# Optimization experiments

Measured on AMD Instinct MI355X. Metric: run time of the kernel, lower is better.

Reference implementation:

```python
import jax, jax.numpy as jnp
import numpy as np

N = 384          # item_num (text regions)
TD = 768         # text hidden (bert-base)
VD = 768         # vision hidden (vit-base)
CD = TD + VD     # commu_dim = 1536
FF = 2048        # TransformerEncoderLayer default dim_feedforward
H = 4            # nhead
L = 2            # num_layers per encoder
EPS = 1e-5


def _enc_params(key, d, scale=0.02):
    ks = jax.random.split(key, 6)
    return dict(
        qkv_w=jax.random.normal(ks[0], (L, 3 * d, d), jnp.float32) * scale,
        qkv_b=jnp.zeros((L, 3 * d), jnp.float32),
        out_w=jax.random.normal(ks[1], (L, d, d), jnp.float32) * scale,
        out_b=jnp.zeros((L, d), jnp.float32),
        ln1_s=jnp.ones((L, d), jnp.float32),
        ln1_b=jnp.zeros((L, d), jnp.float32),
        ff1_w=jax.random.normal(ks[2], (L, FF, d), jnp.float32) * scale,
        ff1_b=jnp.zeros((L, FF), jnp.float32),
        ff2_w=jax.random.normal(ks[3], (L, d, FF), jnp.float32) * scale,
        ff2_b=jnp.zeros((L, d), jnp.float32),
        ln2_s=jnp.ones((L, d), jnp.float32),
        ln2_b=jnp.zeros((L, d), jnp.float32),
    )


def setup_inputs() -> dict:
    key = jax.random.key(0)
    k = jax.random.split(key, 6)
    inp = {
        'text_emb': jax.random.normal(k[0], (N, TD), jnp.float32),
        'vision_emb': jax.random.normal(k[1], (N, VD), jnp.float32),
        'gt_matrix': jax.random.randint(k[2], (N, N), 0, 2, jnp.int32),
    }
    for pref, kk, d in (('t_', k[3], TD), ('c_', k[4], CD)):
        for name, v in _enc_params(kk, d).items():
            inp[pref + name] = v
    inp['lin_w'] = jax.random.normal(k[5], (2, 2 * CD), jnp.float32) * 0.02
    inp['lin_b'] = jnp.zeros((2,), jnp.float32)
    return inp


def _ln(x, s, b):
    m = jnp.mean(x, -1, keepdims=True)
    v = jnp.mean((x - m) ** 2, -1, keepdims=True)
    return (x - m) * jax.lax.rsqrt(v + EPS) * s + b


def _encoder(x, qkv_w, qkv_b, out_w, out_b, ln1_s, ln1_b,
             ff1_w, ff1_b, ff2_w, ff2_b, ln2_s, ln2_b):
    # PyTorch post-norm TransformerEncoder, relu activation, eval mode (no dropout)
    d = x.shape[-1]
    hd = d // H
    for l in range(qkv_w.shape[0]):
        qkv = x @ qkv_w[l].T + qkv_b[l]
        q, kk, v = jnp.split(qkv, 3, axis=-1)
        q = q.reshape(-1, H, hd)
        kk = kk.reshape(-1, H, hd)
        v = v.reshape(-1, H, hd)
        scores = jnp.einsum('qhd,khd->hqk', q, kk) / jnp.sqrt(jnp.float32(hd))
        attn = jax.nn.softmax(scores, -1)
        o = jnp.einsum('hqk,khd->qhd', attn, v).reshape(-1, d)
        x = _ln(x + o @ out_w[l].T + out_b[l], ln1_s[l], ln1_b[l])
        h = jax.nn.relu(x @ ff1_w[l].T + ff1_b[l]) @ ff2_w[l].T + ff2_b[l]
        x = _ln(x + h, ln2_s[l], ln2_b[l])
    return x


def reference(text_emb, vision_emb, gt_matrix,
              t_qkv_w, t_qkv_b, t_out_w, t_out_b, t_ln1_s, t_ln1_b,
              t_ff1_w, t_ff1_b, t_ff2_w, t_ff2_b, t_ln2_s, t_ln2_b,
              c_qkv_w, c_qkv_b, c_out_w, c_out_b, c_ln1_s, c_ln1_b,
              c_ff1_w, c_ff1_b, c_ff2_w, c_ff2_b, c_ln2_s, c_ln2_b,
              lin_w, lin_b):
    te = _encoder(text_emb, t_qkv_w, t_qkv_b, t_out_w, t_out_b, t_ln1_s, t_ln1_b,
                  t_ff1_w, t_ff1_b, t_ff2_w, t_ff2_b, t_ln2_s, t_ln2_b)
    all_emb = jnp.concatenate([te, vision_emb], axis=1)  # [N, CD]
    all_emb = _encoder(all_emb, c_qkv_w, c_qkv_b, c_out_w, c_out_b, c_ln1_s, c_ln1_b,
                       c_ff1_w, c_ff1_b, c_ff2_w, c_ff2_b, c_ln2_s, c_ln2_b)
    # organize(): linear(cat(e_i, e_j)) decomposes exactly as e_i@Wa^T + e_j@Wb^T + b,
    # avoiding the O(N^2 * 2*CD) pair tensor while computing identical math.
    a = all_emb @ lin_w[:, :CD].T + lin_b      # [N, 2]
    c = all_emb @ lin_w[:, CD:].T              # [N, 2]
    logits = a[:, None, :] + c[None, :, :]     # [N, N, 2]
    probs = jax.nn.softmax(logits, -1)         # self.activate(self.linear(...))
    # classificaiton_loss: sum_i CrossEntropyLoss(probs[i], gt[i])  (CE takes probs as logits)
    ls = jax.nn.log_softmax(probs, -1)
    cell = -jnp.take_along_axis(ls, gt_matrix[..., None].astype(jnp.int32), axis=-1)[..., 0]
    cls_loss = jnp.sum(jnp.mean(cell, axis=1))
    # enter_exit_loss over first N-1 items
    link = probs[:, :, 1]
    ee_loss = jnp.sum(jnp.abs(link.sum(1)[:-1] + link.sum(0)[:-1] - 1.0))
    return probs, cls_loss, ee_loss
```

## Files before the change

### kernel.cpp

```cpp
#include <hip/hip_runtime.h>
#include <hip/hip_bf16.h>
#include <math.h>

#define NTOK 384
#define HEADS 4

typedef __attribute__((ext_vector_type(8))) short bf16x8;
typedef __attribute__((ext_vector_type(4))) float f32x4;

__device__ __forceinline__ unsigned short f2b(float f) {
    union { float f; unsigned int u; } v; v.f = f;
    unsigned int r = (v.u + 0x7fff + ((v.u >> 16) & 1)) >> 16;
    return (unsigned short)r;
}

__device__ __forceinline__ void g2l16(const void* g, void* l) {
    __builtin_amdgcn_global_load_lds(
        (const __attribute__((address_space(1))) unsigned int*)g,
        (__attribute__((address_space(3))) unsigned int*)l, 16, 0, 0);
}

__device__ __forceinline__ void stage64(
    const unsigned short* __restrict__ g, int row0, int k0, int ld,
    char* region, int wid, int lane)
{
    int c = wid * 64 + lane;
    int row = c >> 2, p = c & 3;
    int kc = (p - (row >> 1)) & 3;
    g2l16(g + (long)(row0 + row) * ld + k0 + kc * 8,
          region + (wid * 64) * 16);
}

__global__ __launch_bounds__(256, 4) void gemm64(
    const unsigned short* __restrict__ A, const unsigned short* __restrict__ B,
    const float* __restrict__ bias, void* __restrict__ Cv,
    int K, int lda, int ldb, int ldc,
    long sA, long sB, long sC, int relu, int out_bf16,
    unsigned short* __restrict__ vt, int dv2)
{
    __shared__ char smem[2][16384];
    A += (long)blockIdx.z * sA;
    B += (long)blockIdx.z * sB;
    const int t = threadIdx.x, lane = t & 63, wid = t >> 6;
    const int wm = wid >> 1, wn = wid & 1;
    const int r16 = lane & 15, quad = lane >> 4;
    const int row0 = blockIdx.y * 64, col0 = blockIdx.x * 64;

    f32x4 acc[2][2] = {};

    stage64(A, row0,  0, lda, smem[0],         wid, lane);
    stage64(A, row0, 32, lda, smem[0] +  4096, wid, lane);
    stage64(B, col0,  0, ldb, smem[0] +  8192, wid, lane);
    stage64(B, col0, 32, ldb, smem[0] + 12288, wid, lane);
    int buf = 0;

    for (int k0 = 0; k0 < K; k0 += 64) {
        __syncthreads();
        if (k0 + 64 < K) {
            stage64(A, row0, k0 + 64, lda, smem[buf ^ 1],         wid, lane);
            stage64(A, row0, k0 + 96, lda, smem[buf ^ 1] +  4096, wid, lane);
            stage64(B, col0, k0 + 64, ldb, smem[buf ^ 1] +  8192, wid, lane);
            stage64(B, col0, k0 + 96, ldb, smem[buf ^ 1] + 12288, wid, lane);
        }
        const char* cb = smem[buf];
        #pragma unroll
        for (int h = 0; h < 2; ++h) {
            bf16x8 af[2], bfv[2];
            #pragma unroll
            for (int rt = 0; rt < 2; ++rt) {
                int row = wm * 32 + rt * 16 + r16;
                int p = (quad + (row >> 1)) & 3;
                af[rt] = *reinterpret_cast<const bf16x8*>(
                    cb + h * 4096 + row * 64 + p * 16);
            }
            #pragma unroll
            for (int ct = 0; ct < 2; ++ct) {
                int col = wn * 32 + ct * 16 + r16;
                int p = (quad + (col >> 1)) & 3;
                bfv[ct] = *reinterpret_cast<const bf16x8*>(
                    cb + 8192 + h * 4096 + col * 64 + p * 16);
            }
            #pragma unroll
            for (int rt = 0; rt < 2; ++rt)
                #pragma unroll
                for (int ct = 0; ct < 2; ++ct)
                    acc[rt][ct] = __builtin_amdgcn_mfma_f32_16x16x32_bf16(
                        af[rt], bfv[ct], acc[rt][ct], 0, 0, 0);
        }
        buf ^= 1;
    }

    float* Cf = (float*)Cv;
    unsigned short* Cb = (unsigned short*)Cv;
    const long zoff = (long)blockIdx.z * sC;
    const int vwrite = (vt != nullptr) && (col0 >= dv2);
    #pragma unroll
    for (int rt = 0; rt < 2; ++rt) {
        #pragma unroll
        for (int ct = 0; ct < 2; ++ct) {
            f32x4 v = acc[rt][ct];
            int col = col0 + wn * 32 + ct * 16 + r16;
            float bi = bias ? bias[col] : 0.f;
            #pragma unroll
            for (int i = 0; i < 4; ++i) {
                v[i] += bi;
                if (relu) v[i] = fmaxf(v[i], 0.f);
            }
            int rbase = row0 + wm * 32 + rt * 16 + quad * 4;
            if (vwrite) {
                ushort4 p;
                p.x = f2b(v[0]); p.y = f2b(v[1]); p.z = f2b(v[2]); p.w = f2b(v[3]);
                *reinterpret_cast<ushort4*>(vt + (long)(col - dv2) * NTOK + rbase) = p;
            } else if (out_bf16) {
                #pragma unroll
                for (int i = 0; i < 4; ++i)
                    Cb[zoff + (long)(rbase + i) * ldc + col] = f2b(v[i]);
            } else {
                #pragma unroll
                for (int i = 0; i < 4; ++i)
                    Cf[zoff + (long)(rbase + i) * ldc + col] = v[i];
            }
        }
    }
}

#define WO0 0u
#define WO1 3538944u
#define WO2 4718592u
#define WO3 7864320u
#define WO4 11010048u
#define WO5 25165824u
#define WO6 29884416u
#define WO7 36175872u
#define WTOT 42467328u

__global__ __launch_bounds__(256) void convert_weights(
    const float* __restrict__ s0, const float* __restrict__ s1,
    const float* __restrict__ s2, const float* __restrict__ s3,
    const float* __restrict__ s4, const float* __restrict__ s5,
    const float* __restrict__ s6, const float* __restrict__ s7,
    unsigned short* __restrict__ dst)
{
    unsigned int e = (blockIdx.x * 256u + threadIdx.x) * 8u;
    if (e >= WTOT) return;
    const float* src; unsigned int local;
    if      (e < WO1) { src = s0; local = e - WO0; }
    else if (e < WO2) { src = s1; local = e - WO1; }
    else if (e < WO3) { src = s2; local = e - WO2; }
    else if (e < WO4) { src = s3; local = e - WO3; }
    else if (e < WO5) { src = s4; local = e - WO4; }
    else if (e < WO6) { src = s5; local = e - WO5; }
    else if (e < WO7) { src = s6; local = e - WO6; }
    else              { src = s7; local = e - WO7; }
    float4 v0 = *reinterpret_cast<const float4*>(src + local);
    float4 v1 = *reinterpret_cast<const float4*>(src + local + 4);
    uint4 o;
    o.x = (unsigned)f2b(v0.x) | ((unsigned)f2b(v0.y) << 16);
    o.y = (unsigned)f2b(v0.z) | ((unsigned)f2b(v0.w) << 16);
    o.z = (unsigned)f2b(v1.x) | ((unsigned)f2b(v1.y) << 16);
    o.w = (unsigned)f2b(v1.z) | ((unsigned)f2b(v1.w) << 16);
    *reinterpret_cast<uint4*>(dst + e) = o;
}

__global__ __launch_bounds__(64) void softmax_rows(
    const float* __restrict__ S, unsigned short* __restrict__ P, float scale)
{
    const float* p = S + (long)blockIdx.x * NTOK;
    unsigned short* q = P + (long)blockIdx.x * NTOK;
    const int t = threadIdx.x;
    float vals[6];
    float vmax = -1e30f;
    #pragma unroll
    for (int i = 0; i < 6; ++i) {
        vals[i] = p[t + i * 64] * scale;
        vmax = fmaxf(vmax, vals[i]);
    }
    for (int off = 32; off; off >>= 1) vmax = fmaxf(vmax, __shfl_down(vmax, off));
    vmax = __shfl(vmax, 0);
    float sum = 0.f;
    #pragma unroll
    for (int i = 0; i < 6; ++i) { vals[i] = __expf(vals[i] - vmax); sum += vals[i]; }
    for (int off = 32; off; off >>= 1) sum += __shfl_down(sum, off);
    sum = __shfl(sum, 0);
    float inv = 1.f / sum;
    #pragma unroll
    for (int i = 0; i < 6; ++i) q[t + i * 64] = f2b(vals[i] * inv);
}

__global__ __launch_bounds__(256) void add_ln(
    float* __restrict__ x, unsigned short* __restrict__ xb,
    const float* __restrict__ y,
    const float* __restrict__ s, const float* __restrict__ b, int d)
{
    float* xr = x + (long)blockIdx.x * d;
    unsigned short* xbr = xb + (long)blockIdx.x * d;
    const float* yr = y + (long)blockIdx.x * d;
    const int t = threadIdx.x;
    float s1 = 0.f, s2 = 0.f;
    for (int i = t; i < d; i += 256) {
        float v = xr[i] + yr[i];
        s1 += v; s2 += v * v;
    }
    for (int off = 32; off; off >>= 1) { s1 += __shfl_down(s1, off); s2 += __shfl_down(s2, off); }
    __shared__ float r1[4], r2[4];
    int w = t >> 6;
    if ((t & 63) == 0) { r1[w] = s1; r2[w] = s2; }
    __syncthreads();
    if (t == 0) {
        float a = 0.f, c = 0.f;
        for (int i = 0; i < 4; ++i) { a += r1[i]; c += r2[i]; }
        r1[0] = a; r2[0] = c;
    }
    __syncthreads();
    float mean = r1[0] / d;
    float var = r2[0] / d - mean * mean;
    float rstd = rsqrtf(var + 1e-5f);
    for (int i = t; i < d; i += 256) {
        float v = (xr[i] + yr[i] - mean) * rstd * s[i] + b[i];
        xr[i] = v;
        xbr[i] = f2b(v);
    }
}

__global__ void initx_k(const float* __restrict__ src, float* __restrict__ dst,
                        unsigned short* __restrict__ dstb, int n)
{
    int i = blockIdx.x * blockDim.x + threadIdx.x;
    if (i < n) { float v = src[i]; dst[i] = v; dstb[i] = f2b(v); }
}

__global__ void concat_k(const float* __restrict__ te, const float* __restrict__ ve,
                         float* __restrict__ all, unsigned short* __restrict__ allb)
{
    int i = blockIdx.x * blockDim.x + threadIdx.x;
    if (i >= NTOK * 1536) return;
    int r = i / 1536, c = i % 1536;
    float v = (c < 768) ? te[r * 768 + c] : ve[r * 768 + (c - 768)];
    all[i] = v;
    allb[i] = f2b(v);
}

__global__ __launch_bounds__(256) void head_ac(
    const float* __restrict__ all, const float* __restrict__ lin_w,
    const float* __restrict__ lin_b, float* __restrict__ a, float* __restrict__ c)
{
    const int i = blockIdx.x, t = threadIdx.x;
    const float* xr = all + (long)i * 1536;
    float s0 = 0.f, s1 = 0.f, s2 = 0.f, s3 = 0.f;
    for (int e = t; e < 1536; e += 256) {
        float v = xr[e];
        s0 += v * lin_w[e];
        s1 += v * lin_w[3072 + e];
        s2 += v * lin_w[1536 + e];
        s3 += v * lin_w[4608 + e];
    }
    for (int off = 32; off; off >>= 1) {
        s0 += __shfl_down(s0, off); s1 += __shfl_down(s1, off);
        s2 += __shfl_down(s2, off); s3 += __shfl_down(s3, off);
    }
    __shared__ float r[4][4];
    int w = t >> 6;
    if ((t & 63) == 0) { r[0][w] = s0; r[1][w] = s1; r[2][w] = s2; r[3][w] = s3; }
    __syncthreads();
    if (t == 0) {
        float t0 = 0.f, t1 = 0.f, t2 = 0.f, t3 = 0.f;
        for (int k = 0; k < 4; ++k) { t0 += r[0][k]; t1 += r[1][k]; t2 += r[2][k]; t3 += r[3][k]; }
        a[i * 2 + 0] = t0 + lin_b[0];
        a[i * 2 + 1] = t1 + lin_b[1];
        c[i * 2 + 0] = t2;
        c[i * 2 + 1] = t3;
    }
}

__global__ __launch_bounds__(384) void head_probs(
    const float* __restrict__ a, const float* __restrict__ c,
    const int* __restrict__ gt, float* __restrict__ probs,
    float* __restrict__ rowsum, float* __restrict__ rowcell)
{
    const int i = blockIdx.x, j = threadIdx.x;
    float l0 = a[i * 2 + 0] + c[j * 2 + 0];
    float l1 = a[i * 2 + 1] + c[j * 2 + 1];
    float m = fmaxf(l0, l1);
    float e0 = __expf(l0 - m), e1 = __expf(l1 - m);
    float inv = 1.f / (e0 + e1);
    float p0 = e0 * inv, p1 = e1 * inv;
    long base = ((long)i * NTOK + j) * 2;
    probs[base] = p0;
    probs[base + 1] = p1;
    float m2 = fmaxf(p0, p1);
    float z = m2 + __logf(__expf(p0 - m2) + __expf(p1 - m2));
    int g = gt[i * NTOK + j];
    float cell = z - (g ? p1 : p0);
    float cs = cell, ps = p1;
    for (int off = 32; off; off >>= 1) { cs += __shfl_down(cs, off); ps += __shfl_down(ps, off); }
    __shared__ float rc[6], rs[6];
    int w = j >> 6;
    if ((j & 63) == 0) { rc[w] = cs; rs[w] = ps; }
    __syncthreads();
    if (j == 0) {
        float csum = 0.f, psum = 0.f;
        for (int k = 0; k < 6; ++k) { csum += rc[k]; psum += rs[k]; }
        rowcell[i] = csum * (1.f / NTOK);
        rowsum[i] = psum;
    }
}

__global__ __launch_bounds__(64) void colsum_k(const float* __restrict__ probs,
                                               float* __restrict__ colsum)
{
    const int j = blockIdx.x, t = threadIdx.x;
    float s = 0.f;
    for (int i = t; i < NTOK; i += 64)
        s += probs[((long)i * NTOK + j) * 2 + 1];
    for (int off = 32; off; off >>= 1) s += __shfl_down(s, off);
    if (t == 0) colsum[j] = s;
}

__global__ __launch_bounds__(384) void finalize_k(
    const float* __restrict__ rowcell, const float* __restrict__ rowsum,
    const float* __restrict__ colsum, float* __restrict__ out)
{
    const int t = threadIdx.x;
    float cls = rowcell[t];
    float ee = (t < NTOK - 1) ? fabsf(rowsum[t] + colsum[t] - 1.f) : 0.f;
    for (int off = 32; off; off >>= 1) { cls += __shfl_down(cls, off); ee += __shfl_down(ee, off); }
    __shared__ float rc[6], re[6];
    int w = t >> 6;
    if ((t & 63) == 0) { rc[w] = cls; re[w] = ee; }
    __syncthreads();
    if (t == 0) {
        float a = 0.f, b = 0.f;
        for (int k = 0; k < 6; ++k) { a += rc[k]; b += re[k]; }
        out[NTOK * NTOK * 2 + 0] = a;
        out[NTOK * NTOK * 2 + 1] = b;
    }
}

static void run_encoder(float* x, unsigned short* xb, int d,
                        const unsigned short* wq, const unsigned short* wo,
                        const unsigned short* w1, const unsigned short* w2,
                        const float* qkv_b, const float* out_b,
                        const float* ln1_s, const float* ln1_b,
                        const float* ff1_b, const float* ff2_b,
                        const float* ln2_s, const float* ln2_b,
                        unsigned short* qkvb, float* sc, unsigned short* attnb,
                        unsigned short* vtb, unsigned short* ob,
                        unsigned short* t1b, float* t2,
                        hipStream_t stream)
{
    const int dq = 3 * d;
    const int hd = d / HEADS;
    const float scale = 1.0f / sqrtf((float)hd);
    for (int l = 0; l < 2; ++l) {
        gemm64<<<dim3(dq / 64, 6), 256, 0, stream>>>(
            xb, wq + (long)l * dq * d, qkv_b + l * dq, qkvb,
            d, d, d, dq, 0, 0, 0, 0, 1, vtb, 2 * d);
        gemm64<<<dim3(6, 6, HEADS), 256, 0, stream>>>(
            qkvb, qkvb + d, nullptr, sc,
            hd, dq, dq, NTOK, (long)hd, (long)hd, (long)NTOK * NTOK,
            0, 0, nullptr, 0);
        softmax_rows<<<HEADS * NTOK, 64, 0, stream>>>(sc, attnb, scale);
        gemm64<<<dim3(hd / 64, 6, HEADS), 256, 0, stream>>>(
            attnb, vtb, nullptr, ob,
            NTOK, NTOK, NTOK, d, (long)NTOK * NTOK, (long)hd * NTOK, (long)hd,
            0, 1, nullptr, 0);
        gemm64<<<dim3(d / 64, 6), 256, 0, stream>>>(
            ob, wo + (long)l * d * d, out_b + l * d, t2,
            d, d, d, d, 0, 0, 0, 0, 0, nullptr, 0);
        add_ln<<<NTOK, 256, 0, stream>>>(x, xb, t2, ln1_s + l * d, ln1_b + l * d, d);
        gemm64<<<dim3(2048 / 64, 6), 256, 0, stream>>>(
            xb, w1 + (long)l * 2048 * d, ff1_b + l * 2048, t1b,
            d, d, d, 2048, 0, 0, 0, 1, 1, nullptr, 0);
        gemm64<<<dim3(d / 64, 6), 256, 0, stream>>>(
            t1b, w2 + (long)l * d * 2048, ff2_b + l * d, t2,
            2048, 2048, 2048, d, 0, 0, 0, 0, 0, nullptr, 0);
        add_ln<<<NTOK, 256, 0, stream>>>(x, xb, t2, ln2_s + l * d, ln2_b + l * d, d);
    }
}

extern "C" void kernel_launch(void* const* d_in, const int* in_sizes, int n_in,
                              void* d_out, int out_size, void* d_ws, size_t ws_size,
                              hipStream_t stream)
{
    const float* text_emb   = (const float*)d_in[0];
    const float* vision_emb = (const float*)d_in[1];
    const int*   gt         = (const int*)  d_in[2];
    const float* t_qkv_w = (const float*)d_in[3];
    const float* t_qkv_b = (const float*)d_in[4];
    const float* t_out_w = (const float*)d_in[5];
    const float* t_out_b = (const float*)d_in[6];
    const float* t_ln1_s = (const float*)d_in[7];
    const float* t_ln1_b = (const float*)d_in[8];
    const float* t_ff1_w = (const float*)d_in[9];
    const float* t_ff1_b = (const float*)d_in[10];
    const float* t_ff2_w = (const float*)d_in[11];
    const float* t_ff2_b = (const float*)d_in[12];
    const float* t_ln2_s = (const float*)d_in[13];
    const float* t_ln2_b = (const float*)d_in[14];
    const float* c_qkv_w = (const float*)d_in[15];
    const float* c_qkv_b = (const float*)d_in[16];
    const float* c_out_w = (const float*)d_in[17];
    const float* c_out_b = (const float*)d_in[18];
    const float* c_ln1_s = (const float*)d_in[19];
    const float* c_ln1_b = (const float*)d_in[20];
    const float* c_ff1_w = (const float*)d_in[21];
    const float* c_ff1_b = (const float*)d_in[22];
    const float* c_ff2_w = (const float*)d_in[23];
    const float* c_ff2_b = (const float*)d_in[24];
    const float* c_ln2_s = (const float*)d_in[25];
    const float* c_ln2_b = (const float*)d_in[26];
    const float* lin_w   = (const float*)d_in[27];
    const float* lin_b   = (const float*)d_in[28];
    float* out = (float*)d_out;

    float* ws = (float*)d_ws;
    float* xt      = ws;
    float* all     = xt + 294912;
    float* t2      = all + 589824;
    float* sc      = t2 + 589824;
    float* abuf    = sc + 589824;
    float* cbuf    = abuf + 768;
    float* rowsum  = cbuf + 768;
    float* rowcell = rowsum + 384;
    float* colsum  = rowcell + 384;
    unsigned short* ub = (unsigned short*)(ws + 2067072);
    unsigned short* xtb   = ub;
    unsigned short* allb  = xtb + 294912;
    unsigned short* qkvb  = allb + 589824;
    unsigned short* attnb = qkvb + 1769472;
    unsigned short* vtb   = attnb + 589824;
    unsigned short* ob    = vtb + 589824;
    unsigned short* t1b   = ob + 589824;
    unsigned short* wb    = t1b + 786432;

    convert_weights<<<(WTOT / 8 + 255) / 256, 256, 0, stream>>>(
        t_qkv_w, t_out_w, t_ff1_w, t_ff2_w,
        c_qkv_w, c_out_w, c_ff1_w, c_ff2_w, wb);

    initx_k<<<(294912 + 255) / 256, 256, 0, stream>>>(text_emb, xt, xtb, 294912);
    run_encoder(xt, xtb, 768,
                wb + WO0, wb + WO1, wb + WO2, wb + WO3,
                t_qkv_b, t_out_b, t_ln1_s, t_ln1_b,
                t_ff1_b, t_ff2_b, t_ln2_s, t_ln2_b,
                qkvb, sc, attnb, vtb, ob, t1b, t2, stream);

    concat_k<<<(589824 + 255) / 256, 256, 0, stream>>>(xt, vision_emb, all, allb);
    run_encoder(all, allb, 1536,
                wb + WO4, wb + WO5, wb + WO6, wb + WO7,
                c_qkv_b, c_out_b, c_ln1_s, c_ln1_b,
                c_ff1_b, c_ff2_b, c_ln2_s, c_ln2_b,
                qkvb, sc, attnb, vtb, ob, t1b, t2, stream);

    head_ac<<<NTOK, 256, 0, stream>>>(all, lin_w, lin_b, abuf, cbuf);
    head_probs<<<NTOK, 384, 0, stream>>>(abuf, cbuf, gt, out, rowsum, rowcell);
    colsum_k<<<NTOK, 64, 0, stream>>>(out, colsum);
    finalize_k<<<1, 384, 0, stream>>>(rowcell, rowsum, colsum, out);
}
```

Measured before the change: 563.9 us.

## Triple-buffer GEMM LDS staging with explicit vmcnt waits

Changes the 64x64 bf16 GEMM from a double-buffered to a triple-buffered LDS pipeline, prefetching two k-tiles ahead. It replaces __syncthreads with targeted s_waitcnt vmcnt counts plus s_barrier, so the in-flight global-to-LDS loads for the next tile are not drained each iteration. LDS per block grows to 48KB and launch bounds drop from 4 to 3 blocks per CU, which may reduce occupancy.

```diff
diff --git a/kernel.cpp b/kernel.cpp
--- a/kernel.cpp
+++ b/kernel.cpp
@@ -31,14 +31,26 @@
           region + (wid * 64) * 16);
 }
 
-__global__ __launch_bounds__(256, 4) void gemm64(
+__device__ __forceinline__ void stage_tile(
+    const unsigned short* __restrict__ A, const unsigned short* __restrict__ B,
+    int row0, int col0, int k0, int lda, int ldb,
+    char* buf, int wid, int lane)
+{
+    stage64(A, row0, k0,      lda, buf,         wid, lane);
+    stage64(A, row0, k0 + 32, lda, buf +  4096, wid, lane);
+    stage64(B, col0, k0,      ldb, buf +  8192, wid, lane);
+    stage64(B, col0, k0 + 32, ldb, buf + 12288, wid, lane);
+    __builtin_amdgcn_sched_barrier(0);
+}
+
+__global__ __launch_bounds__(256, 3) void gemm64(
     const unsigned short* __restrict__ A, const unsigned short* __restrict__ B,
     const float* __restrict__ bias, void* __restrict__ Cv,
     int K, int lda, int ldb, int ldc,
     long sA, long sB, long sC, int relu, int out_bf16,
     unsigned short* __restrict__ vt, int dv2)
 {
-    __shared__ char smem[2][16384];
+    __shared__ char smem[3][16384];
     A += (long)blockIdx.z * sA;
     B += (long)blockIdx.z * sB;
     const int t = threadIdx.x, lane = t & 63, wid = t >> 6;
@@ -47,22 +59,24 @@
     const int row0 = blockIdx.y * 64, col0 = blockIdx.x * 64;
 
     f32x4 acc[2][2] = {};
-
-    stage64(A, row0,  0, lda, smem[0],         wid, lane);
-    stage64(A, row0, 32, lda, smem[0] +  4096, wid, lane);
-    stage64(B, col0,  0, ldb, smem[0] +  8192, wid, lane);
-    stage64(B, col0, 32, ldb, smem[0] + 12288, wid, lane);
-    int buf = 0;
-
-    for (int k0 = 0; k0 < K; k0 += 64) {
-        __syncthreads();
-        if (k0 + 64 < K) {
-            stage64(A, row0, k0 + 64, lda, smem[buf ^ 1],         wid, lane);
-            stage64(A, row0, k0 + 96, lda, smem[buf ^ 1] +  4096, wid, lane);
-            stage64(B, col0, k0 + 64, ldb, smem[buf ^ 1] +  8192, wid, lane);
-            stage64(B, col0, k0 + 96, ldb, smem[buf ^ 1] + 12288, wid, lane);
+    const int NT = K >> 6;
+
+    stage_tile(A, B, row0, col0, 0, lda, ldb, smem[0], wid, lane);
+    if (NT > 1)
+        stage_tile(A, B, row0, col0, 64, lda, ldb, smem[1], wid, lane);
+
+    int cur = 0, sb = 2;
+    for (int kt = 0; kt < NT; ++kt) {
+        if (kt + 1 < NT) asm volatile("s_waitcnt vmcnt(4)" ::: "memory");
+        else             asm volatile("s_waitcnt vmcnt(0) lgkmcnt(0)" ::: "memory");
+        __builtin_amdgcn_s_barrier();
+        if (kt + 2 < NT) {
+            stage_tile(A, B, row0, col0, (kt + 2) * 64, lda, ldb,
+                       smem[sb], wid, lane);
+            sb = (sb == 2) ? 0 : sb + 1;
         }
-        const char* cb = smem[buf];
+        const char* cb = smem[cur];
+        cur = (cur == 2) ? 0 : cur + 1;
         #pragma unroll
         for (int h = 0; h < 2; ++h) {
             bf16x8 af[2], bfv[2];
@@ -87,7 +101,6 @@
                     acc[rt][ct] = __builtin_amdgcn_mfma_f32_16x16x32_bf16(
                         af[rt], bfv[ct], acc[rt][ct], 0, 0, 0);
         }
-        buf ^= 1;
     }
 
     float* Cf = (float*)Cv;
```

Result: faster. 501.8 us (-11.0%).
